# Kernel optimization log

Measured on AMD Instinct MI355X. Metric: run time of the kernel, lower is better.

## Reference

```python
import jax, jax.numpy as jnp
import numpy as np

B, F, H, D, TE, CE = 16384, 1024, 64, 256, 4, 4

def setup_inputs() -> dict:
    key = jax.random.key(0)
    ks = iter(jax.random.split(key, 40))
    s = 0.02
    mk = lambda shape: jax.random.normal(next(ks), shape, jnp.float32) * s
    inp = {
        'x_A': jax.random.normal(next(ks), (B, F), jnp.float32),
        'x_S': jax.random.normal(next(ks), (B, F), jnp.float32),
        'x_B': jax.random.normal(next(ks), (B, F), jnp.float32),
        # stacked per-expert weights for the three expert groups (A, Shared, B)
        'W1A': mk((TE, F, H)), 'b1A': mk((TE, H)), 'W2A': mk((TE, H, D)), 'b2A': mk((TE, D)),
        'W1S': mk((CE, F, H)), 'b1S': mk((CE, H)), 'W2S': mk((CE, H, D)), 'b2S': mk((CE, D)),
        'W1B': mk((TE, F, H)), 'b1B': mk((TE, H)), 'W2B': mk((TE, H, D)), 'b2B': mk((TE, D)),
        # gate weights
        'WgA': mk((F, TE + CE)), 'bgA': mk((TE + CE,)),
        'WgB': mk((F, TE + CE)), 'bgB': mk((TE + CE,)),
        'WgS': mk((F, 2 * TE + CE)), 'bgS': mk((2 * TE + CE,)),
    }
    return inp

def _expert_group(x, W1, b1, W2, b2):
    # x: [B,F], W1: [E,F,H] -> [B,E,H]; W2: [E,H,D] -> [B,E,D]
    h = jax.nn.relu(jnp.einsum('bf,efh->beh', x, W1) + b1)  # dropout p=0 -> identity
    return jax.nn.relu(jnp.einsum('beh,ehd->bed', h, W2) + b2)

def reference(x_A, x_S, x_B,
              W1A, b1A, W2A, b2A,
              W1S, b1S, W2S, b2S,
              W1B, b1B, W2B, b2B,
              WgA, bgA, WgB, bgB, WgS, bgS):
    EA = _expert_group(x_A, W1A, b1A, W2A, b2A)  # [B,TE,D]
    ES = _expert_group(x_S, W1S, b1S, W2S, b2S)  # [B,CE,D]
    EB = _expert_group(x_B, W1B, b1B, W2B, b2B)  # [B,TE,D]
    gA = jax.nn.softmax(x_A @ WgA + bgA, axis=1)  # [B,TE+CE]
    gS = jax.nn.softmax(x_S @ WgS + bgS, axis=1)  # [B,2TE+CE]
    gB = jax.nn.softmax(x_B @ WgB + bgB, axis=1)  # [B,TE+CE]
    outA = jnp.einsum('bed,be->bd', jnp.concatenate([EA, ES], axis=1), gA)
    outS = jnp.einsum('bed,be->bd', jnp.concatenate([EA, ES, EB], axis=1), gS)
    outB = jnp.einsum('bed,be->bd', jnp.concatenate([EB, ES], axis=1), gB)
    return (outA, outS, outB)
```

## Files before the change

### kernel.cpp

```cpp
#include <hip/hip_runtime.h>


#define BB 16384
#define FF 1024

typedef _Float16 f16;
typedef __fp16 h16x2 __attribute__((ext_vector_type(2)));
typedef _Float16 f16x8 __attribute__((ext_vector_type(8)));
typedef float f32x4 __attribute__((ext_vector_type(4)));

__device__ __forceinline__ void load_lds16(const void* g, void* l) {
    __builtin_amdgcn_global_load_lds(
        (const __attribute__((address_space(1))) unsigned int*)g,
        (__attribute__((address_space(3))) unsigned int*)l, 16, 0, 0);
}

__device__ __forceinline__ f16x8 pack8(float4 lo, float4 hi) {
    union { f16x8 v; h16x2 p[4]; } u;
    u.p[0] = __builtin_amdgcn_cvt_pkrtz(lo.x, lo.y);
    u.p[1] = __builtin_amdgcn_cvt_pkrtz(lo.z, lo.w);
    u.p[2] = __builtin_amdgcn_cvt_pkrtz(hi.x, hi.y);
    u.p[3] = __builtin_amdgcn_cvt_pkrtz(hi.z, hi.w);
    return u.v;
}

__global__ __launch_bounds__(256) void pack_kernel(
    const float* __restrict__ W1A, const float* __restrict__ W1S, const float* __restrict__ W1B,
    const float* __restrict__ W2A, const float* __restrict__ W2S, const float* __restrict__ W2B,
    const float* __restrict__ WgA, const float* __restrict__ WgS, const float* __restrict__ WgB,
    f16* __restrict__ Wp, f16* __restrict__ W2T, f16* __restrict__ Gp2)
{
    int idx = blockIdx.x * 256 + threadIdx.x;
    if (idx < 786432) {
        int g = idx / 262144, rem = idx % 262144;
        int c = rem >> 10, k = rem & 1023;
        const float* W1 = (g == 0) ? W1A : ((g == 1) ? W1S : W1B);
        Wp[idx] = (f16)W1[((c >> 6) << 16) + k * 64 + (c & 63)];
    } else if (idx < 983040) {
        int j = idx - 786432;
        int g = j / 65536, rem = j % 65536;
        int e = rem >> 14, rr = rem & 16383;
        int d = rr >> 6, hh = rr & 63;
        const float* W2 = (g == 0) ? W2A : ((g == 1) ? W2S : W2B);
        W2T[j] = (f16)W2[e * 16384 + hh * 256 + d];
    } else {
        int j = idx - 983040;
        int g = j / 16384, rem = j % 16384;
        int c = rem >> 10, k = rem & 1023;
        int ng = (g == 1) ? 12 : 8;
        const float* Wg = (g == 0) ? WgA : ((g == 1) ? WgS : WgB);
        Gp2[j] = (c < ng) ? (f16)Wg[k * ng + c] : (f16)0.0f;
    }
}

__global__ __launch_bounds__(512, 4) void l1_kernel(
    const float* __restrict__ xA, const float* __restrict__ xS, const float* __restrict__ xB,
    const float* __restrict__ b1A, const float* __restrict__ b1S, const float* __restrict__ b1B,
    const float* __restrict__ bgA, const float* __restrict__ bgS, const float* __restrict__ bgB,
    const f16* __restrict__ Wp,
    const f16* __restrict__ Gp2,
    f16* __restrict__ hbuf,
    float* __restrict__ gates)
{
    const int g = blockIdx.y;
    const float* x  = (g == 0) ? xA  : ((g == 1) ? xS  : xB);
    const float* b1 = (g == 0) ? b1A : ((g == 1) ? b1S : b1B);
    const float* bg = (g == 0) ? bgA : ((g == 1) ? bgS : bgB);
    const int ng = (g == 1) ? 12 : 8;
    float* gout = gates + ((g == 0) ? (size_t)0
                         : (g == 1) ? (size_t)BB * 8
                                    : (size_t)BB * 8 + (size_t)BB * 12);

    const int row0 = blockIdx.x * 128;

    __shared__ __align__(16) float Asf[2][128 * 32];
    __shared__ __align__(16) f16   Bsh[2][256 * 32];

    const int tid  = threadIdx.x;
    const int lane = tid & 63;
    const int wave = tid >> 6;
    const int wm = (wave >> 2) * 64;
    const int wn = (wave & 3) * 64;
    const int lrow = lane & 15;
    const int quad = lane >> 4;
    const bool my_gate = ((wave & 3) == 0);

    const f16* Wgrp = Wp + (size_t)g * 256 * 1024;
    const f16* Ggrp = Gp2 + ((size_t)g * 16 + lrow) * 1024 + quad * 8;
    const float* xrow = x + (size_t)row0 * FF;

    f32x4 acc[4][4] = {};
    f32x4 gacc[4] = {};

#pragma unroll
    for (int r = 0; r < 2; ++r) {
        int s = r * 512 + tid;
        int m = s >> 3, slot = s & 7;
        int seg = slot ^ (m & 7);
        load_lds16(xrow + (size_t)m * FF + seg * 4, &Asf[0][s * 4]);
    }
#pragma unroll
    for (int r = 0; r < 2; ++r) {
        int s = r * 512 + tid;
        int n = s >> 2, slot = s & 3;
        int seg = slot ^ ((n >> 1) & 3);
        load_lds16(Wgrp + (size_t)n * FF + seg * 8, &Bsh[0][s * 8]);
    }

    int cur = 0;
    for (int k0 = 0; k0 < FF; k0 += 32) {
        __syncthreads();
        int nxt = cur ^ 1;
        if (k0 + 32 < FF) {
#pragma unroll
            for (int r = 0; r < 2; ++r) {
                int s = r * 512 + tid;
                int m = s >> 3, slot = s & 7;
                int seg = slot ^ (m & 7);
                load_lds16(xrow + (size_t)m * FF + (k0 + 32) + seg * 4, &Asf[nxt][s * 4]);
            }
#pragma unroll
            for (int r = 0; r < 2; ++r) {
                int s = r * 512 + tid;
                int n = s >> 2, slot = s & 3;
                int seg = slot ^ ((n >> 1) & 3);
                load_lds16(Wgrp + (size_t)n * FF + (k0 + 32) + seg * 8, &Bsh[nxt][s * 8]);
            }
        }

        f16x8 gb;
        if (my_gate) gb = *(const f16x8*)(Ggrp + k0);

        f16x8 af[4];
#pragma unroll
        for (int i = 0; i < 4; ++i) {
            int m = wm + i * 16 + lrow;
            const float* rp = &Asf[cur][m * 32];
            int s0 = (2 * quad) ^ (m & 7);
            float4 lo = *(const float4*)(rp + s0 * 4);
            float4 hi = *(const float4*)(rp + (s0 ^ 1) * 4);
            af[i] = pack8(lo, hi);
        }
#pragma unroll
        for (int j = 0; j < 4; ++j) {
            int n = wn + j * 16 + lrow;
            int slot = quad ^ ((n >> 1) & 3);
            f16x8 bf = *(const f16x8*)(&Bsh[cur][n * 32 + slot * 8]);
#pragma unroll
            for (int i = 0; i < 4; ++i)
                acc[i][j] = __builtin_amdgcn_mfma_f32_16x16x32_f16(af[i], bf, acc[i][j], 0, 0, 0);
        }
        if (my_gate) {
#pragma unroll
            for (int i = 0; i < 4; ++i)
                gacc[i] = __builtin_amdgcn_mfma_f32_16x16x32_f16(af[i], gb, gacc[i], 0, 0, 0);
        }
        cur = nxt;
    }

#pragma unroll
    for (int j = 0; j < 4; ++j) {
        int c = wn + j * 16 + lrow;
        float bias = b1[c];
#pragma unroll
        for (int i = 0; i < 4; ++i) {
#pragma unroll
            for (int r = 0; r < 4; ++r) {
                int row = row0 + wm + i * 16 + quad * 4 + r;
                float v = fmaxf(acc[i][j][r] + bias, 0.0f);
                hbuf[((size_t)g * BB + row) * 256 + c] = (f16)v;
            }
        }
    }

    if (my_gate) {
        int c = lrow;
        bool valid = (c < ng);
        float bias = valid ? bg[c] : 0.0f;
#pragma unroll
        for (int i = 0; i < 4; ++i) {
#pragma unroll
            for (int r = 0; r < 4; ++r) {
                int row = row0 + wm + i * 16 + quad * 4 + r;
                float logit = valid ? (gacc[i][r] + bias) : -1e30f;
                float mx = logit;
#pragma unroll
                for (int m = 1; m < 16; m <<= 1)
                    mx = fmaxf(mx, __shfl_xor(mx, m, 16));
                float ev = valid ? __expf(logit - mx) : 0.0f;
                float sum = ev;
#pragma unroll
                for (int m = 1; m < 16; m <<= 1)
                    sum += __shfl_xor(sum, m, 16);
                if (valid) gout[(size_t)row * ng + c] = ev / sum;
            }
        }
    }
}

__global__ __launch_bounds__(512) void l2_kernel(
    const f16* __restrict__ hbuf,
    const f16* __restrict__ W2T,
    const float* __restrict__ b2A, const float* __restrict__ b2S, const float* __restrict__ b2B,
    const float* __restrict__ gates,
    float* __restrict__ out)
{
    const int o = blockIdx.y;
    const int row0 = blockIdx.x * 64;
    const int tid = threadIdx.x;
    const int lane = tid & 63;
    const int wave = tid >> 6;
    const int wm = (wave >> 2) * 32;
    const int wn = (wave & 3) * 64;
    const int lrow = lane & 15;
    const int quad = lane >> 4;

    const int ng = (o == 1) ? 12 : 8;
    const float* gp = gates + ((o == 0) ? (size_t)0
                             : (o == 1) ? (size_t)BB * 8
                                        : (size_t)BB * 8 + (size_t)BB * 12);

    __shared__ float gsh[64 * 12];
    for (int idx = tid; idx < 64 * ng; idx += 512)
        gsh[idx] = gp[(size_t)(row0 + idx / ng) * ng + (idx % ng)];
    __syncthreads();

    f32x4 oacc[2][4] = {};

    for (int k = 0; k < ng; ++k) {
        int e = k & 3, gi;
        if (o == 0)      gi = (k < 4) ? 0 : 1;
        else if (o == 1) gi = k >> 2;
        else             gi = (k < 4) ? 2 : 1;

        const f16* hs = hbuf + ((size_t)gi * BB + row0 + wm) * 256 + e * 64;
        const f16* w2 = W2T + (size_t)(gi * 4 + e) * 256 * 64;
        const float* b2 = (gi == 0) ? b2A : ((gi == 1) ? b2S : b2B);

        f16x8 af[2][2];
#pragma unroll
        for (int i = 0; i < 2; ++i)
#pragma unroll
            for (int kk = 0; kk < 2; ++kk)
                af[i][kk] = *(const f16x8*)(hs + (size_t)(i * 16 + lrow) * 256 + kk * 32 + quad * 8);

#pragma unroll
        for (int j = 0; j < 4; ++j) {
            int d = wn + j * 16 + lrow;
            f16x8 bf0 = *(const f16x8*)(w2 + (size_t)d * 64 + quad * 8);
            f16x8 bf1 = *(const f16x8*)(w2 + (size_t)d * 64 + 32 + quad * 8);
            float bias = b2[e * 256 + d];
#pragma unroll
            for (int i = 0; i < 2; ++i) {
                f32x4 t = {};
                t = __builtin_amdgcn_mfma_f32_16x16x32_f16(af[i][0], bf0, t, 0, 0, 0);
                t = __builtin_amdgcn_mfma_f32_16x16x32_f16(af[i][1], bf1, t, 0, 0, 0);
#pragma unroll
                for (int r = 0; r < 4; ++r) {
                    int rl = wm + i * 16 + quad * 4 + r;
                    float v = fmaxf(t[r] + bias, 0.0f);
                    oacc[i][j][r] += gsh[rl * ng + k] * v;
                }
            }
        }
    }

#pragma unroll
    for (int j = 0; j < 4; ++j) {
        int d = wn + j * 16 + lrow;
#pragma unroll
        for (int i = 0; i < 2; ++i) {
#pragma unroll
            for (int r = 0; r < 4; ++r) {
                int rl = wm + i * 16 + quad * 4 + r;
                out[((size_t)o * BB + row0 + rl) * 256 + d] = oacc[i][j][r];
            }
        }
    }
}

extern "C" void kernel_launch(void* const* d_in, const int* in_sizes, int n_in,
                              void* d_out, int out_size, void* d_ws, size_t ws_size,
                              hipStream_t stream)
{
    (void)in_sizes; (void)n_in; (void)out_size; (void)ws_size;

    const float* xA  = (const float*)d_in[0];
    const float* xS  = (const float*)d_in[1];
    const float* xB  = (const float*)d_in[2];
    const float* W1A = (const float*)d_in[3];
    const float* b1A = (const float*)d_in[4];
    const float* W2A = (const float*)d_in[5];
    const float* b2A = (const float*)d_in[6];
    const float* W1S = (const float*)d_in[7];
    const float* b1S = (const float*)d_in[8];
    const float* W2S = (const float*)d_in[9];
    const float* b2S = (const float*)d_in[10];
    const float* W1B = (const float*)d_in[11];
    const float* b1B = (const float*)d_in[12];
    const float* W2B = (const float*)d_in[13];
    const float* b2B = (const float*)d_in[14];
    const float* WgA = (const float*)d_in[15];
    const float* bgA = (const float*)d_in[16];
    const float* WgB = (const float*)d_in[17];
    const float* bgB = (const float*)d_in[18];
    const float* WgS = (const float*)d_in[19];
    const float* bgS = (const float*)d_in[20];

    char* ws = (char*)d_ws;
    f16*   Wp   = (f16*)(ws);
    f16*   W2T  = (f16*)(ws + 0x180000);
    f16*   Gp2  = (f16*)(ws + 0x1E0000);
    f16*   hbuf = (f16*)(ws + 0x200000);
    float* gate = (float*)(ws + 0x200000 + 0x1800000);

    pack_kernel<<<4032, 256, 0, stream>>>(W1A, W1S, W1B, W2A, W2S, W2B,
                                          WgA, WgS, WgB, Wp, W2T, Gp2);
    l1_kernel<<<dim3(128, 3), 512, 0, stream>>>(
        xA, xS, xB, b1A, b1S, b1B, bgA, bgS, bgB,
        Wp, Gp2, hbuf, gate);
    l2_kernel<<<dim3(256, 3), 512, 0, stream>>>(
        hbuf, W2T, b2A, b2S, b2B, gate, (float*)d_out);
}
```

Before: 366.8 us.

## Pre-swizzle weights into MFMA fragment order and restage L1/L2 operand loading

The pack kernel now writes W1 and W2 in per-lane MFMA fragment order, so the B operands load straight from global memory (L2-cached) and the B tiles in LDS go away. In L1, x is loaded into registers, converted to fp16 once per element and stored to a smaller fp16 LDS tile. This replaces repeated fp32 LDS reads followed by per-wave conversion. L2 now processes 128 rows per block, double-buffers the hidden activations in a swizzled LDS tile and gives each wave a wider 128-column slice. The trade-off is more register pressure in L2 and unshared global weight loads in every wave.

```diff
diff --git a/kernel.cpp b/kernel.cpp
--- a/kernel.cpp
+++ b/kernel.cpp
@@ -24,32 +24,46 @@
     return u.v;
 }
 
+__device__ __forceinline__ int expert_gi(int o, int k) {
+    if (o == 0) return (k < 4) ? 0 : 1;
+    if (o == 1) return k >> 2;
+    return (k < 4) ? 2 : 1;
+}
+
 __global__ __launch_bounds__(256) void pack_kernel(
     const float* __restrict__ W1A, const float* __restrict__ W1S, const float* __restrict__ W1B,
     const float* __restrict__ W2A, const float* __restrict__ W2S, const float* __restrict__ W2B,
     const float* __restrict__ WgA, const float* __restrict__ WgS, const float* __restrict__ WgB,
-    f16* __restrict__ Wp, f16* __restrict__ W2T, f16* __restrict__ Gp2)
+    f16* __restrict__ W1F, f16* __restrict__ W2F, f16* __restrict__ Gp2)
 {
     int idx = blockIdx.x * 256 + threadIdx.x;
     if (idx < 786432) {
-        int g = idx / 262144, rem = idx % 262144;
-        int c = rem >> 10, k = rem & 1023;
+        int g = idx / 262144, r = idx % 262144;
+        int nt = r >> 14, r2 = r & 16383;
+        int kt = r2 >> 9, s = r2 & 511;
+        int lane = s >> 3, j = s & 7;
+        int c = nt * 16 + (lane & 15);
+        int k = kt * 32 + (lane >> 4) * 8 + j;
         const float* W1 = (g == 0) ? W1A : ((g == 1) ? W1S : W1B);
-        Wp[idx] = (f16)W1[((c >> 6) << 16) + k * 64 + (c & 63)];
+        W1F[idx] = (f16)W1[((c >> 6) << 16) + k * 64 + (c & 63)];
     } else if (idx < 983040) {
-        int j = idx - 786432;
-        int g = j / 65536, rem = j % 65536;
-        int e = rem >> 14, rr = rem & 16383;
-        int d = rr >> 6, hh = rr & 63;
+        int t = idx - 786432;
+        int g = t / 65536, r = t % 65536;
+        int e = r >> 14, r2 = r & 16383;
+        int nt = r2 >> 10, r3 = r2 & 1023;
+        int kt = r3 >> 9, s = r3 & 511;
+        int lane = s >> 3, j = s & 7;
+        int d = nt * 16 + (lane & 15);
+        int hh = kt * 32 + (lane >> 4) * 8 + j;
         const float* W2 = (g == 0) ? W2A : ((g == 1) ? W2S : W2B);
-        W2T[j] = (f16)W2[e * 16384 + hh * 256 + d];
+        W2F[t] = (f16)W2[e * 16384 + hh * 256 + d];
     } else {
-        int j = idx - 983040;
-        int g = j / 16384, rem = j % 16384;
+        int t = idx - 983040;
+        int g = t / 16384, rem = t % 16384;
         int c = rem >> 10, k = rem & 1023;
         int ng = (g == 1) ? 12 : 8;
         const float* Wg = (g == 0) ? WgA : ((g == 1) ? WgS : WgB);
-        Gp2[j] = (c < ng) ? (f16)Wg[k * ng + c] : (f16)0.0f;
+        Gp2[t] = (c < ng) ? (f16)Wg[k * ng + c] : (f16)0.0f;
     }
 }
 
@@ -57,7 +71,7 @@
     const float* __restrict__ xA, const float* __restrict__ xS, const float* __restrict__ xB,
     const float* __restrict__ b1A, const float* __restrict__ b1S, const float* __restrict__ b1B,
     const float* __restrict__ bgA, const float* __restrict__ bgS, const float* __restrict__ bgB,
-    const f16* __restrict__ Wp,
+    const f16* __restrict__ W1F,
     const f16* __restrict__ Gp2,
     f16* __restrict__ hbuf,
     float* __restrict__ gates)
@@ -73,8 +87,7 @@
 
     const int row0 = blockIdx.x * 128;
 
-    __shared__ __align__(16) float Asf[2][128 * 32];
-    __shared__ __align__(16) f16   Bsh[2][256 * 32];
+    __shared__ __align__(16) f16 Ash[2][128 * 32];
 
     const int tid  = threadIdx.x;
     const int lane = tid & 63;
@@ -85,77 +98,52 @@
     const int quad = lane >> 4;
     const bool my_gate = ((wave & 3) == 0);
 
-    const f16* Wgrp = Wp + (size_t)g * 256 * 1024;
-    const f16* Ggrp = Gp2 + ((size_t)g * 16 + lrow) * 1024 + quad * 8;
-    const float* xrow = x + (size_t)row0 * FF;
+    const f16* Wbase = W1F + (size_t)g * 262144;
+    const f16* Ggrp  = Gp2 + ((size_t)g * 16 + lrow) * 1024 + quad * 8;
+
+    const int am = tid >> 2;
+    const int ac = tid & 3;
+    const float* xld = x + (size_t)(row0 + am) * FF + ac * 8;
+    const int aoff = am * 32 + ac * 8;
 
     f32x4 acc[4][4] = {};
     f32x4 gacc[4] = {};
 
-#pragma unroll
-    for (int r = 0; r < 2; ++r) {
-        int s = r * 512 + tid;
-        int m = s >> 3, slot = s & 7;
-        int seg = slot ^ (m & 7);
-        load_lds16(xrow + (size_t)m * FF + seg * 4, &Asf[0][s * 4]);
-    }
-#pragma unroll
-    for (int r = 0; r < 2; ++r) {
-        int s = r * 512 + tid;
-        int n = s >> 2, slot = s & 3;
-        int seg = slot ^ ((n >> 1) & 3);
-        load_lds16(Wgrp + (size_t)n * FF + seg * 8, &Bsh[0][s * 8]);
-    }
-
-    int cur = 0;
-    for (int k0 = 0; k0 < FF; k0 += 32) {
+    {
+        float4 lo = *(const float4*)(xld);
+        float4 hi = *(const float4*)(xld + 4);
+        *(f16x8*)(&Ash[0][aoff]) = pack8(lo, hi);
+    }
+    __syncthreads();
+
+    for (int kt = 0; kt < 32; ++kt) {
+        const int cur = kt & 1, nxt = cur ^ 1;
+        float4 lo, hi;
+        if (kt < 31) {
+            lo = *(const float4*)(xld + (kt + 1) * 32);
+            hi = *(const float4*)(xld + (kt + 1) * 32 + 4);
+        }
+        f16x8 gb;
+        if (my_gate) gb = *(const f16x8*)(Ggrp + kt * 32);
+
+        f16x8 bf[4];
+#pragma unroll
+        for (int j = 0; j < 4; ++j) {
+            int nt = (wn >> 4) + j;
+            bf[j] = *(const f16x8*)(Wbase + ((size_t)nt * 32 + kt) * 512 + lane * 8);
+        }
+#pragma unroll
+        for (int i = 0; i < 4; ++i) {
+            f16x8 a = *(const f16x8*)(&Ash[cur][(wm + i * 16 + lrow) * 32 + quad * 8]);
+#pragma unroll
+            for (int j = 0; j < 4; ++j)
+                acc[i][j] = __builtin_amdgcn_mfma_f32_16x16x32_f16(a, bf[j], acc[i][j], 0, 0, 0);
+            if (my_gate)
+                gacc[i] = __builtin_amdgcn_mfma_f32_16x16x32_f16(a, gb, gacc[i], 0, 0, 0);
+        }
+        if (kt < 31)
+            *(f16x8*)(&Ash[nxt][aoff]) = pack8(lo, hi);
         __syncthreads();
-        int nxt = cur ^ 1;
-        if (k0 + 32 < FF) {
-#pragma unroll
-            for (int r = 0; r < 2; ++r) {
-                int s = r * 512 + tid;
-                int m = s >> 3, slot = s & 7;
-                int seg = slot ^ (m & 7);
-                load_lds16(xrow + (size_t)m * FF + (k0 + 32) + seg * 4, &Asf[nxt][s * 4]);
-            }
-#pragma unroll
-            for (int r = 0; r < 2; ++r) {
-                int s = r * 512 + tid;
-                int n = s >> 2, slot = s & 3;
-                int seg = slot ^ ((n >> 1) & 3);
-                load_lds16(Wgrp + (size_t)n * FF + (k0 + 32) + seg * 8, &Bsh[nxt][s * 8]);
-            }
-        }
-
-        f16x8 gb;
-        if (my_gate) gb = *(const f16x8*)(Ggrp + k0);
-
-        f16x8 af[4];
-#pragma unroll
-        for (int i = 0; i < 4; ++i) {
-            int m = wm + i * 16 + lrow;
-            const float* rp = &Asf[cur][m * 32];
-            int s0 = (2 * quad) ^ (m & 7);
-            float4 lo = *(const float4*)(rp + s0 * 4);
-            float4 hi = *(const float4*)(rp + (s0 ^ 1) * 4);
-            af[i] = pack8(lo, hi);
-        }
-#pragma unroll
-        for (int j = 0; j < 4; ++j) {
-            int n = wn + j * 16 + lrow;
-            int slot = quad ^ ((n >> 1) & 3);
-            f16x8 bf = *(const f16x8*)(&Bsh[cur][n * 32 + slot * 8]);
-#pragma unroll
-            for (int i = 0; i < 4; ++i)
-                acc[i][j] = __builtin_amdgcn_mfma_f32_16x16x32_f16(af[i], bf, acc[i][j], 0, 0, 0);
-        }
-        if (my_gate) {
-#pragma unroll
-            for (int i = 0; i < 4; ++i)
-                gacc[i] = __builtin_amdgcn_mfma_f32_16x16x32_f16(af[i], gb, gacc[i], 0, 0, 0);
-        }
-        cur = nxt;
     }
 
 #pragma unroll
@@ -198,20 +186,20 @@
     }
 }
 
-__global__ __launch_bounds__(512) void l2_kernel(
+__global__ __launch_bounds__(512, 4) void l2_kernel(
     const f16* __restrict__ hbuf,
-    const f16* __restrict__ W2T,
+    const f16* __restrict__ W2F,
     const float* __restrict__ b2A, const float* __restrict__ b2S, const float* __restrict__ b2B,
     const float* __restrict__ gates,
     float* __restrict__ out)
 {
     const int o = blockIdx.y;
-    const int row0 = blockIdx.x * 64;
+    const int row0 = blockIdx.x * 128;
     const int tid = threadIdx.x;
     const int lane = tid & 63;
     const int wave = tid >> 6;
-    const int wm = (wave >> 2) * 32;
-    const int wn = (wave & 3) * 64;
+    const int wm = (wave >> 1) * 32;
+    const int wn = (wave & 1) * 128;
     const int lrow = lane & 15;
     const int quad = lane >> 4;
 
@@ -220,35 +208,64 @@
                              : (o == 1) ? (size_t)BB * 8
                                         : (size_t)BB * 8 + (size_t)BB * 12);
 
-    __shared__ float gsh[64 * 12];
-    for (int idx = tid; idx < 64 * ng; idx += 512)
+    __shared__ __align__(16) f16 Ash[2][128 * 64];
+    __shared__ float gsh[128 * 12];
+
+    for (int idx = tid; idx < 128 * ng; idx += 512)
         gsh[idx] = gp[(size_t)(row0 + idx / ng) * ng + (idx % ng)];
-    __syncthreads();
-
-    f32x4 oacc[2][4] = {};
+
+    {
+        int gi = expert_gi(o, 0);
+        const f16* hs = hbuf + ((size_t)gi * BB + row0) * 256;
+#pragma unroll
+        for (int r = 0; r < 2; ++r) {
+            int s = r * 512 + tid;
+            int m = s >> 3, slot = s & 7;
+            int chunk = slot ^ (m & 7);
+            load_lds16(hs + (size_t)m * 256 + chunk * 8, &Ash[0][s * 8]);
+        }
+    }
+
+    f32x4 oacc[2][8] = {};
 
     for (int k = 0; k < ng; ++k) {
-        int e = k & 3, gi;
-        if (o == 0)      gi = (k < 4) ? 0 : 1;
-        else if (o == 1) gi = k >> 2;
-        else             gi = (k < 4) ? 2 : 1;
-
-        const f16* hs = hbuf + ((size_t)gi * BB + row0 + wm) * 256 + e * 64;
-        const f16* w2 = W2T + (size_t)(gi * 4 + e) * 256 * 64;
+        const int cur = k & 1, nxt = cur ^ 1;
+        __syncthreads();
+
+        if (k + 1 < ng) {
+            int gi2 = expert_gi(o, k + 1);
+            int e2 = (k + 1) & 3;
+            const f16* hs = hbuf + ((size_t)gi2 * BB + row0) * 256 + e2 * 64;
+#pragma unroll
+            for (int r = 0; r < 2; ++r) {
+                int s = r * 512 + tid;
+                int m = s >> 3, slot = s & 7;
+                int chunk = slot ^ (m & 7);
+                load_lds16(hs + (size_t)m * 256 + chunk * 8, &Ash[nxt][s * 8]);
+            }
+        }
+
+        const int e = k & 3;
+        const int gi = expert_gi(o, k);
         const float* b2 = (gi == 0) ? b2A : ((gi == 1) ? b2S : b2B);
+        const f16* wb = W2F + (size_t)(gi * 4 + e) * 16384;
 
         f16x8 af[2][2];
 #pragma unroll
-        for (int i = 0; i < 2; ++i)
-#pragma unroll
-            for (int kk = 0; kk < 2; ++kk)
-                af[i][kk] = *(const f16x8*)(hs + (size_t)(i * 16 + lrow) * 256 + kk * 32 + quad * 8);
-
-#pragma unroll
-        for (int j = 0; j < 4; ++j) {
+        for (int i = 0; i < 2; ++i) {
+#pragma unroll
+            for (int kk = 0; kk < 2; ++kk) {
+                int m = wm + i * 16 + lrow;
+                int slot = (kk * 4 + quad) ^ (m & 7);
+                af[i][kk] = *(const f16x8*)(&Ash[cur][m * 64 + slot * 8]);
+            }
+        }
+#pragma unroll
+        for (int j = 0; j < 8; ++j) {
+            int nt = (wn >> 4) + j;
+            f16x8 bf0 = *(const f16x8*)(wb + ((size_t)nt * 2 + 0) * 512 + lane * 8);
+            f16x8 bf1 = *(const f16x8*)(wb + ((size_t)nt * 2 + 1) * 512 + lane * 8);
             int d = wn + j * 16 + lrow;
-            f16x8 bf0 = *(const f16x8*)(w2 + (size_t)d * 64 + quad * 8);
-            f16x8 bf1 = *(const f16x8*)(w2 + (size_t)d * 64 + 32 + quad * 8);
             float bias = b2[e * 256 + d];
 #pragma unroll
             for (int i = 0; i < 2; ++i) {
@@ -266,7 +283,7 @@
     }
 
 #pragma unroll
-    for (int j = 0; j < 4; ++j) {
+    for (int j = 0; j < 8; ++j) {
         int d = wn + j * 16 + lrow;
 #pragma unroll
         for (int i = 0; i < 2; ++i) {
@@ -308,17 +325,17 @@
     const float* bgS = (const float*)d_in[20];
 
     char* ws = (char*)d_ws;
-    f16*   Wp   = (f16*)(ws);
-    f16*   W2T  = (f16*)(ws + 0x180000);
+    f16*   W1F  = (f16*)(ws);
+    f16*   W2F  = (f16*)(ws + 0x180000);
     f16*   Gp2  = (f16*)(ws + 0x1E0000);
     f16*   hbuf = (f16*)(ws + 0x200000);
     float* gate = (float*)(ws + 0x200000 + 0x1800000);
 
     pack_kernel<<<4032, 256, 0, stream>>>(W1A, W1S, W1B, W2A, W2S, W2B,
-                                          WgA, WgS, WgB, Wp, W2T, Gp2);
+                                          WgA, WgS, WgB, W1F, W2F, Gp2);
     l1_kernel<<<dim3(128, 3), 512, 0, stream>>>(
         xA, xS, xB, b1A, b1S, b1B, bgA, bgS, bgB,
-        Wp, Gp2, hbuf, gate);
-    l2_kernel<<<dim3(256, 3), 512, 0, stream>>>(
-        hbuf, W2T, b2A, b2S, b2B, gate, (float*)d_out);
-}
+        W1F, Gp2, hbuf, gate);
+    l2_kernel<<<dim3(128, 3), 512, 0, stream>>>(
+        hbuf, W2F, b2A, b2S, b2B, gate, (float*)d_out);
+}
```

Result: faster. 342.4 us (-6.6%).
